# Optimization experiments

Hardware: AMD Instinct MI355X
Metric: run time of the kernel (lower is better)

## Reference

```python
import jax, jax.numpy as jnp
import numpy as np

N, L, D, H, MLP_MULT = 2, 384, 512, 8, 4
HD = D // H
DM = D * MLP_MULT
EPS = 1e-5


def _linear_params(key, out_dim, in_dim, scale=0.02):
    kw, kb = jax.random.split(key)
    w = jax.random.normal(kw, (out_dim, in_dim), jnp.float32) * scale
    b = jax.random.normal(kb, (out_dim,), jnp.float32) * scale
    return w, b


def setup_inputs() -> dict:
    key = jax.random.key(0)
    ks = jax.random.split(key, 12)
    x = jax.random.normal(ks[0], (N, L, D), jnp.float32)
    mem = jax.random.normal(ks[1], (N, L, D), jnp.float32)
    pairwise_distances = jax.random.normal(ks[2], (N, L, L, D), jnp.float32)
    mem_padding_mask = jax.random.randint(ks[3], (N, L), 0, 2).astype(bool)
    qw, qb = _linear_params(ks[4], D, D)
    kvw, kvb = _linear_params(ks[5], 2 * D, D)
    pw, pb = _linear_params(ks[6], D, D)
    edw, edb = _linear_params(ks[7], H, D)
    w1, b1 = _linear_params(ks[8], DM, D)
    w2, b2 = _linear_params(ks[9], DM, DM)
    w3, b3 = _linear_params(ks[10], D, DM)
    return {
        'x': x, 'mem': mem, 'pairwise_distances': pairwise_distances,
        'mem_padding_mask': mem_padding_mask,
        'qw': qw, 'qb': qb, 'kvw': kvw, 'kvb': kvb, 'pw': pw, 'pb': pb,
        'edw': edw, 'edb': edb,
        'ln1_g': jnp.ones((D,), jnp.float32), 'ln1_b': jnp.zeros((D,), jnp.float32),
        'ln2_g': jnp.ones((D,), jnp.float32), 'ln2_b': jnp.zeros((D,), jnp.float32),
        'w1': w1, 'b1': b1, 'w2': w2, 'b2': b2, 'w3': w3, 'b3': b3,
    }


def _layernorm(x, g, b):
    m = jnp.mean(x, axis=-1, keepdims=True)
    v = jnp.mean((x - m) ** 2, axis=-1, keepdims=True)
    return (x - m) * jax.lax.rsqrt(v + EPS) * g + b


def reference(x, mem, pairwise_distances, mem_padding_mask,
              qw, qb, kvw, kvb, pw, pb, edw, edb,
              ln1_g, ln1_b, ln2_g, ln2_b,
              w1, b1, w2, b2, w3, b3):
    scale = HD ** -0.5
    a_in = _layernorm(x, ln1_g, ln1_b)
    a_mem = _layernorm(mem, ln1_g, ln1_b)

    q = (a_in @ qw.T + qb).reshape(N, L, H, HD).transpose(0, 2, 1, 3)   # (N,H,L1,HD)
    kv = (a_mem @ kvw.T + kvb).reshape(N, L, 2, H, HD)
    k = kv[:, :, 0].transpose(0, 2, 1, 3)                               # (N,H,L2,HD)
    v = kv[:, :, 1].transpose(0, 2, 1, 3)

    scores = jnp.einsum('bhid,bhjd->bhij', q, k) * scale                # (N,H,L1,L2)

    # T5-style relative position bias from pairwise distances
    bias = (pairwise_distances @ edw.T + edb)                            # (N,L1,L2,H)
    scores = scores + bias.transpose(0, 3, 1, 2)

    # padding mask (True = padded); rows that are fully padded get a zero
    # mask instead (then their output is zeroed after attention)
    all_pad = jnp.all(mem_padding_mask, axis=-1)                         # (N,)
    neg_inf = jnp.asarray(-jnp.inf, scores.dtype)
    mask = jnp.where(mem_padding_mask[:, None, None, :], neg_inf, 0.0)
    mask = jnp.where(all_pad[:, None, None, None], 0.0, mask)
    scores = scores + mask

    attn = jax.nn.softmax(scores, axis=-1)
    out = jnp.einsum('bhij,bhjd->bhid', attn, v)                         # (N,H,L1,HD)
    out = out * (~all_pad)[:, None, None, None]
    out = out.transpose(0, 2, 1, 3).reshape(N, L, D)

    x = x + (out @ pw.T + pb)

    h = _layernorm(x, ln2_g, ln2_b)
    h = jax.nn.silu(h @ w1.T + b1)
    h = jax.nn.silu(h @ w2.T + b2)
    h = h @ w3.T + b3
    return x + h
```

## Files before the change

### kernel.cpp

```cpp
#include <hip/hip_runtime.h>
#include <hip/hip_bf16.h>
#include <math.h>

#define NB   2
#define LSEQ 384
#define DMODEL 512
#define NH   8
#define HD2  64
#define DMLP 2048
#define LL2  (LSEQ*LSEQ)
#define ROWS (NB*LSEQ)

#define BIAS_BLOCKS (NB * LL2 / 64)
#define LN_BLOCKS   384
#define CVT_BLOCKS  1024

using bf16x8 = __attribute__((ext_vector_type(8))) short;
using f32x4  = __attribute__((ext_vector_type(4))) float;

__device__ __forceinline__ unsigned short f2bf(float f) {
    union { __hip_bfloat16 h; unsigned short u; } cv;
    cv.h = __float2bfloat16(f);
    return cv.u;
}
__device__ __forceinline__ float bf2f(unsigned short u) {
    union { float f; unsigned int i; } c;
    c.i = ((unsigned int)u) << 16;
    return c.f;
}

__device__ __forceinline__ void gload_lds16(const void* g, void* l) {
    __builtin_amdgcn_global_load_lds(
        (const __attribute__((address_space(1))) void*)g,
        (__attribute__((address_space(3))) void*)l, 16, 0, 0);
}

__global__ __launch_bounds__(256) void pre_bias_kernel(
        const float* __restrict__ pd, const unsigned short* __restrict__ edwb_in,
        const float* __restrict__ edb, const int* __restrict__ mask,
        unsigned short* __restrict__ biasb,
        const float* __restrict__ x, const float* __restrict__ mem,
        const float* __restrict__ ln1g, const float* __restrict__ ln1b,
        unsigned short* __restrict__ a_in, unsigned short* __restrict__ a_mem,
        const float* __restrict__ s0, const float* __restrict__ s1,
        const float* __restrict__ s2, const float* __restrict__ s3,
        const float* __restrict__ s4, const float* __restrict__ s5,
        const float* __restrict__ edw,
        unsigned short* __restrict__ d0, unsigned short* __restrict__ d1,
        unsigned short* __restrict__ d2, unsigned short* __restrict__ d3,
        unsigned short* __restrict__ d4, unsigned short* __restrict__ d5,
        unsigned short* __restrict__ edwb_out) {
    __shared__ float Asb[2][64 * 64];
    const int tid = threadIdx.x;

    if (blockIdx.x < BIAS_BLOCKS) {
        const int lane = tid & 63, w = tid >> 6;
        const int T = blockIdx.x;
        const size_t row0 = (size_t)T * 64;
        const int n = T / 2304;
        const int rem64 = (T - n * 2304) * 64;
        const int i = rem64 / LSEQ, j0 = rem64 % LSEQ;

        int pad = 1;
        for (int j = lane; j < LSEQ; j += 64) pad &= (mask[n * LSEQ + j] != 0) ? 1 : 0;
        unsigned long long bal = __ballot(pad);
        const int ap = (bal == ~0ull) ? 1 : 0;

        int rr[4], sc[4];
        #pragma unroll
        for (int q = 0; q < 4; q++) {
            int s = q * 256 + tid;
            rr[q] = s >> 4;
            int cs = s & 15;
            sc[q] = (cs & 8) | ((cs & 7) ^ (rr[q] & 7));
        }

        const int c = lane & 15, g = lane >> 4;
        f32x4 acc = {};

        #pragma unroll
        for (int q = 0; q < 4; q++)
            gload_lds16(pd + (row0 + rr[q]) * DMODEL + sc[q] * 4, &Asb[0][(q * 256 + tid) * 4]);
        __syncthreads();

        for (int kc = 0; kc < 8; kc++) {
            if (kc < 7) {
                const int nb = (kc + 1) & 1;
                #pragma unroll
                for (int q = 0; q < 4; q++)
                    gload_lds16(pd + (row0 + rr[q]) * DMODEL + (kc + 1) * 64 + sc[q] * 4,
                                &Asb[nb][(q * 256 + tid) * 4]);
            }
            const float* Ab = &Asb[kc & 1][0];
            #pragma unroll
            for (int ks = 0; ks < 2; ks++) {
                const int ch0 = (8 * ks) | ((2 * g) ^ (c & 7));
                const int ch1 = (8 * ks) | ((2 * g + 1) ^ (c & 7));
                float4 a0 = *(const float4*)&Ab[(w * 16 + c) * 64 + ch0 * 4];
                float4 a1 = *(const float4*)&Ab[(w * 16 + c) * 64 + ch1 * 4];
                bf16x8 af;
                af[0] = (short)f2bf(a0.x); af[1] = (short)f2bf(a0.y);
                af[2] = (short)f2bf(a0.z); af[3] = (short)f2bf(a0.w);
                af[4] = (short)f2bf(a1.x); af[5] = (short)f2bf(a1.y);
                af[6] = (short)f2bf(a1.z); af[7] = (short)f2bf(a1.w);
                bf16x8 bfv = *(const bf16x8*)&edwb_in[c * 512 + kc * 64 + ks * 32 + g * 8];
                acc = __builtin_amdgcn_mfma_f32_16x16x32_bf16(af, bfv, acc, 0, 0, 0);
            }
            if (kc < 7) __syncthreads();
        }

        if (c < 8) {
            const float eb = edb[c];
            const int jj = j0 + w * 16 + g * 4;
            int4 mv = *(const int4*)&mask[n * LSEQ + jj];
            const float NEGINF = -__builtin_inff();
            ushort4 o;
            o.x = f2bf(acc[0] + eb + ((!ap && mv.x) ? NEGINF : 0.0f));
            o.y = f2bf(acc[1] + eb + ((!ap && mv.y) ? NEGINF : 0.0f));
            o.z = f2bf(acc[2] + eb + ((!ap && mv.z) ? NEGINF : 0.0f));
            o.w = f2bf(acc[3] + eb + ((!ap && mv.w) ? NEGINF : 0.0f));
            *(ushort4*)&biasb[(size_t)(n * 8 + c) * LL2 + (size_t)i * LSEQ + jj] = o;
        }
        return;
    }

    if (blockIdx.x < BIAS_BLOCKS + LN_BLOCKS) {
        int lane = tid & 63;
        int row  = (blockIdx.x - BIAS_BLOCKS) * 4 + (tid >> 6);
        const float* src = (row < ROWS) ? x : mem;
        unsigned short* dst = (row < ROWS) ? a_in : a_mem;
        int r2 = (row < ROWS) ? row : row - ROWS;
        const float* p = src + (size_t)r2 * DMODEL + lane * 8;
        float4 v0 = *(const float4*)p;
        float4 v1 = *(const float4*)(p + 4);
        float s  = v0.x + v0.y + v0.z + v0.w + v1.x + v1.y + v1.z + v1.w;
        float ss = v0.x*v0.x + v0.y*v0.y + v0.z*v0.z + v0.w*v0.w
                 + v1.x*v1.x + v1.y*v1.y + v1.z*v1.z + v1.w*v1.w;
        #pragma unroll
        for (int o = 32; o; o >>= 1) { s += __shfl_xor(s, o); ss += __shfl_xor(ss, o); }
        float m   = s * (1.0f / DMODEL);
        float var = ss * (1.0f / DMODEL) - m * m;
        float r   = rsqrtf(var + 1e-5f);
        float4 g0 = *(const float4*)(ln1g + lane * 8);
        float4 g1 = *(const float4*)(ln1g + lane * 8 + 4);
        float4 b0 = *(const float4*)(ln1b + lane * 8);
        float4 b1 = *(const float4*)(ln1b + lane * 8 + 4);
        unsigned short* q = dst + (size_t)r2 * DMODEL + lane * 8;
        ushort4 lo = {f2bf((v0.x-m)*r*g0.x+b0.x), f2bf((v0.y-m)*r*g0.y+b0.y),
                      f2bf((v0.z-m)*r*g0.z+b0.z), f2bf((v0.w-m)*r*g0.w+b0.w)};
        ushort4 hi = {f2bf((v1.x-m)*r*g1.x+b1.x), f2bf((v1.y-m)*r*g1.y+b1.y),
                      f2bf((v1.z-m)*r*g1.z+b1.z), f2bf((v1.w-m)*r*g1.w+b1.w)};
        *(ushort4*)q = lo;
        *(ushort4*)(q + 4) = hi;
        return;
    }

    const int stride = CVT_BLOCKS * 256;
    const int t0 = (blockIdx.x - BIAS_BLOCKS - LN_BLOCKS) * 256 + tid;
    const float* srcs[6] = {s0, s1, s2, s3, s4, s5};
    unsigned short* dsts[6] = {d0, d1, d2, d3, d4, d5};
    const int nf4[6] = {DMODEL*DMODEL/4, 2*DMODEL*DMODEL/4, DMODEL*DMODEL/4,
                        DMLP*DMODEL/4, DMLP*DMLP/4, DMLP*DMODEL/4};
    #pragma unroll
    for (int a = 0; a < 6; a++) {
        const float* s = srcs[a];
        unsigned short* d = dsts[a];
        for (int i = t0; i < nf4[a]; i += stride) {
            float4 v = *(const float4*)(s + (size_t)i * 4);
            ushort4 o = {f2bf(v.x), f2bf(v.y), f2bf(v.z), f2bf(v.w)};
            *(ushort4*)(d + (size_t)i * 4) = o;
        }
    }
    for (int i = t0; i < 16 * 512 / 4; i += stride) {
        int row = i >> 7;
        float4 v = {0.f, 0.f, 0.f, 0.f};
        if (row < 8) v = *(const float4*)(edw + (size_t)i * 4);
        ushort4 o = {f2bf(v.x), f2bf(v.y), f2bf(v.z), f2bf(v.w)};
        *(ushort4*)(edwb_out + (size_t)i * 4) = o;
    }
}

__global__ void edw_cvt_kernel(const float* __restrict__ edw,
                               unsigned short* __restrict__ edwb) {
    int i = blockIdx.x * 256 + threadIdx.x;
    float4 v = {0.f, 0.f, 0.f, 0.f};
    if (i < 8 * 512 / 4) v = *(const float4*)(edw + (size_t)i * 4);
    ushort4 o = {f2bf(v.x), f2bf(v.y), f2bf(v.z), f2bf(v.w)};
    *(ushort4*)(edwb + (size_t)i * 4) = o;
}

__global__ __launch_bounds__(256) void ln_kernel(const float* __restrict__ src0,
                                                 const float* __restrict__ g,
                                                 const float* __restrict__ b,
                                                 unsigned short* __restrict__ dst0) {
    int lane = threadIdx.x & 63;
    int row  = blockIdx.x * 4 + (threadIdx.x >> 6);
    const float* p = src0 + (size_t)row * DMODEL + lane * 8;
    float4 v0 = *(const float4*)p;
    float4 v1 = *(const float4*)(p + 4);
    float s  = v0.x + v0.y + v0.z + v0.w + v1.x + v1.y + v1.z + v1.w;
    float ss = v0.x*v0.x + v0.y*v0.y + v0.z*v0.z + v0.w*v0.w
             + v1.x*v1.x + v1.y*v1.y + v1.z*v1.z + v1.w*v1.w;
    #pragma unroll
    for (int o = 32; o; o >>= 1) { s += __shfl_xor(s, o); ss += __shfl_xor(ss, o); }
    float m   = s * (1.0f / DMODEL);
    float var = ss * (1.0f / DMODEL) - m * m;
    float r   = rsqrtf(var + 1e-5f);
    float4 g0 = *(const float4*)(g + lane * 8);
    float4 g1 = *(const float4*)(g + lane * 8 + 4);
    float4 b0 = *(const float4*)(b + lane * 8);
    float4 b1 = *(const float4*)(b + lane * 8 + 4);
    unsigned short* q = dst0 + (size_t)row * DMODEL + lane * 8;
    ushort4 lo = {f2bf((v0.x-m)*r*g0.x+b0.x), f2bf((v0.y-m)*r*g0.y+b0.y),
                  f2bf((v0.z-m)*r*g0.z+b0.z), f2bf((v0.w-m)*r*g0.w+b0.w)};
    ushort4 hi = {f2bf((v1.x-m)*r*g1.x+b1.x), f2bf((v1.y-m)*r*g1.y+b1.y),
                  f2bf((v1.z-m)*r*g1.z+b1.z), f2bf((v1.w-m)*r*g1.w+b1.w)};
    *(ushort4*)q = lo;
    *(ushort4*)(q + 4) = hi;
}

template<int ACT, int RES, int OBF>
__device__ __forceinline__ void gemm_body(const unsigned short* __restrict__ A,
        const unsigned short* __restrict__ W, const float* __restrict__ bv,
        const float* __restrict__ Rsd, void* __restrict__ Cv,
        int Nn, int K, int m0, int n0, short* As, short* Ws) {
    const int tid  = threadIdx.x;
    const int lane = tid & 63, w = tid >> 6;
    const int wr = w >> 1, wc = w & 1;
    const int s0 = tid, s1 = 256 + tid;
    const int r0 = s0 >> 3, c0 = ((s0 & 7) ^ (r0 & 7)) << 3;
    const int r1 = s1 >> 3, c1 = ((s1 & 7) ^ (r1 & 7)) << 3;
    const unsigned short* ag0 = A + (size_t)(m0 + r0) * K + c0;
    const unsigned short* ag1 = A + (size_t)(m0 + r1) * K + c1;
    const unsigned short* wg0 = W + (size_t)(n0 + r0) * K + c0;
    const unsigned short* wg1 = W + (size_t)(n0 + r1) * K + c1;

    f32x4 acc[2][2] = {};
    const int lc = lane & 15, lr = lane >> 4;
    const int KT = K >> 6;

    #pragma unroll
    for (int t = 0; t < 4; t++) {
        const int b = t * 4096, k0 = t << 6;
        gload_lds16(ag0 + k0, &As[b + s0 * 8]);
        gload_lds16(ag1 + k0, &As[b + s1 * 8]);
        gload_lds16(wg0 + k0, &Ws[b + s0 * 8]);
        gload_lds16(wg1 + k0, &Ws[b + s1 * 8]);
    }

    for (int t = 0; t < KT; t++) {
        int rem = KT - 1 - t; if (rem > 3) rem = 3;
        if (rem >= 3)      asm volatile("s_waitcnt vmcnt(12)" ::: "memory");
        else if (rem == 2) asm volatile("s_waitcnt vmcnt(8)"  ::: "memory");
        else if (rem == 1) asm volatile("s_waitcnt vmcnt(4)"  ::: "memory");
        else               asm volatile("s_waitcnt vmcnt(0)"  ::: "memory");
        __builtin_amdgcn_s_barrier();
        __builtin_amdgcn_sched_barrier(0);
        const int cur = (t & 3) * 4096;
        bf16x8 af[2][2], bfr[2][2];
        #pragma unroll
        for (int m = 0; m < 2; m++) {
            const int rra = wr * 32 + m * 16 + lc;
            #pragma unroll
            for (int kk = 0; kk < 2; kk++) {
                const int cc = (lr + kk * 4) ^ (rra & 7);
                af[m][kk] = *(const bf16x8*)&As[cur + rra * 64 + cc * 8];
            }
        }
        #pragma unroll
        for (int nn = 0; nn < 2; nn++) {
            const int rrb = wc * 32 + nn * 16 + lc;
            #pragma unroll
            for (int kk = 0; kk < 2; kk++) {
                const int cc = (lr + kk * 4) ^ (rrb & 7);
                bfr[nn][kk] = *(const bf16x8*)&Ws[cur + rrb * 64 + cc * 8];
            }
        }
        #pragma unroll
        for (int m = 0; m < 2; m++)
            #pragma unroll
            for (int nn = 0; nn < 2; nn++) {
                acc[m][nn] = __builtin_amdgcn_mfma_f32_16x16x32_bf16(af[m][0], bfr[nn][0], acc[m][nn], 0, 0, 0);
                acc[m][nn] = __builtin_amdgcn_mfma_f32_16x16x32_bf16(af[m][1], bfr[nn][1], acc[m][nn], 0, 0, 0);
            }
        if (t + 4 < KT) {
            __builtin_amdgcn_sched_barrier(0);
            __builtin_amdgcn_s_barrier();
            const int b = cur, k0 = (t + 4) << 6;
            gload_lds16(ag0 + k0, &As[b + s0 * 8]);
            gload_lds16(ag1 + k0, &As[b + s1 * 8]);
            gload_lds16(wg0 + k0, &Ws[b + s0 * 8]);
            gload_lds16(wg1 + k0, &Ws[b + s1 * 8]);
        }
    }

    #pragma unroll
    for (int nn = 0; nn < 2; nn++) {
        int gcol = n0 + wc * 32 + nn * 16 + lc;
        float bb = bv[gcol];
        #pragma unroll
        for (int m = 0; m < 2; m++) {
            #pragma unroll
            for (int r = 0; r < 4; r++) {
                int grow = m0 + wr * 32 + m * 16 + lr * 4 + r;
                float o = acc[m][nn][r] + bb;
                if (ACT) o = o / (1.0f + expf(-o));
                if (RES) o += Rsd[(size_t)grow * Nn + gcol];
                if (OBF) ((unsigned short*)Cv)[(size_t)grow * Nn + gcol] = f2bf(o);
                else     ((float*)Cv)[(size_t)grow * Nn + gcol] = o;
            }
        }
    }
}

template<int ACT, int RES, int OBF>
__global__ __launch_bounds__(256) void mfma_gemm(const unsigned short* __restrict__ A,
                                                 const unsigned short* __restrict__ W,
                                                 const float* __restrict__ bv,
                                                 const float* __restrict__ Rsd,
                                                 void* __restrict__ Cv, int Nn, int K) {
    __shared__ short As[4 * 4096];
    __shared__ short Ws[4 * 4096];
    gemm_body<ACT, RES, OBF>(A, W, bv, Rsd, Cv, Nn, K, blockIdx.y * 64, blockIdx.x * 64, As, Ws);
}

__global__ __launch_bounds__(256) void qkv_gemm(const unsigned short* __restrict__ a_in,
                                                const unsigned short* __restrict__ a_mem,
                                                const unsigned short* __restrict__ qwb,
                                                const unsigned short* __restrict__ kvwb,
                                                const float* __restrict__ qbv,
                                                const float* __restrict__ kvbv,
                                                float* __restrict__ qbuf,
                                                float* __restrict__ kvbuf) {
    __shared__ short As[4 * 4096];
    __shared__ short Ws[4 * 4096];
    const int bx = blockIdx.x;
    const unsigned short* A; const unsigned short* W; const float* bv; float* C; int Nn, n0;
    if (bx < 8) { A = a_in;  W = qwb;  bv = qbv;  C = qbuf;  Nn = DMODEL;     n0 = bx * 64; }
    else        { A = a_mem; W = kvwb; bv = kvbv; C = kvbuf; Nn = 2 * DMODEL; n0 = (bx - 8) * 64; }
    gemm_body<0, 0, 0>(A, W, bv, nullptr, C, Nn, DMODEL, blockIdx.y * 64, n0, As, Ws);
}

__global__ __launch_bounds__(256) void scores_kernel(const float* __restrict__ q,
                                                     const float* __restrict__ kv,
                                                     const unsigned short* __restrict__ biasb,
                                                     float* __restrict__ S) {
    const int n = blockIdx.z, h = blockIdx.y;
    const int it = blockIdx.x / 12, jt = blockIdx.x % 12;
    __shared__ float Qs[64][32];
    __shared__ float Ks[64][32];
    const int tid = threadIdx.x;
    const int r = tid >> 3, c = (tid & 7) << 3;
    {
        const float* qp = q + ((size_t)(n * LSEQ + it * 32 + r)) * DMODEL + h * HD2 + c;
        float4 q0 = *(const float4*)qp;
        float4 q1 = *(const float4*)(qp + 4);
        Qs[c+0][r]=q0.x; Qs[c+1][r]=q0.y; Qs[c+2][r]=q0.z; Qs[c+3][r]=q0.w;
        Qs[c+4][r]=q1.x; Qs[c+5][r]=q1.y; Qs[c+6][r]=q1.z; Qs[c+7][r]=q1.w;
        const float* kp = kv + ((size_t)(n * LSEQ + jt * 32 + r)) * (2 * DMODEL) + h * HD2 + c;
        float4 k0 = *(const float4*)kp;
        float4 k1 = *(const float4*)(kp + 4);
        Ks[c+0][r]=k0.x; Ks[c+1][r]=k0.y; Ks[c+2][r]=k0.z; Ks[c+3][r]=k0.w;
        Ks[c+4][r]=k1.x; Ks[c+5][r]=k1.y; Ks[c+6][r]=k1.z; Ks[c+7][r]=k1.w;
    }
    __syncthreads();
    const int tx = tid & 15, ty = tid >> 4;
    float acc[2][2] = {{0.f,0.f},{0.f,0.f}};
    #pragma unroll
    for (int k = 0; k < 64; k++) {
        float2 a  = *(const float2*)&Qs[k][ty << 1];
        float2 b2 = *(const float2*)&Ks[k][tx << 1];
        acc[0][0] = fmaf(a.x, b2.x, acc[0][0]);
        acc[0][1] = fmaf(a.x, b2.y, acc[0][1]);
        acc[1][0] = fmaf(a.y, b2.x, acc[1][0]);
        acc[1][1] = fmaf(a.y, b2.y, acc[1][1]);
    }
    #pragma unroll
    for (int i2 = 0; i2 < 2; i2++) {
        int gi = it * 32 + (ty << 1) + i2;
        int gj = jt * 32 + (tx << 1);
        size_t idx = ((size_t)(n * 8 + h)) * LL2 + (size_t)gi * LSEQ + gj;
        ushort2 bb = *(const ushort2*)&biasb[idx];
        S[idx]     = acc[i2][0] * 0.125f + bf2f(bb.x);
        S[idx + 1] = acc[i2][1] * 0.125f + bf2f(bb.y);
    }
}

__global__ __launch_bounds__(256) void softmax_kernel(float* __restrict__ S) {
    int lane = threadIdx.x & 63;
    int row  = blockIdx.x * 4 + (threadIdx.x >> 6);
    float* p = S + (size_t)row * LSEQ;
    float v[6];
    #pragma unroll
    for (int cc = 0; cc < 6; cc++) v[cc] = p[cc * 64 + lane];
    float mx = v[0];
    #pragma unroll
    for (int cc = 1; cc < 6; cc++) mx = fmaxf(mx, v[cc]);
    #pragma unroll
    for (int o = 32; o; o >>= 1) mx = fmaxf(mx, __shfl_xor(mx, o));
    float sum = 0.f;
    #pragma unroll
    for (int cc = 0; cc < 6; cc++) { v[cc] = __expf(v[cc] - mx); sum += v[cc]; }
    #pragma unroll
    for (int o = 32; o; o >>= 1) sum += __shfl_xor(sum, o);
    float inv = 1.0f / sum;
    #pragma unroll
    for (int cc = 0; cc < 6; cc++) p[cc * 64 + lane] = v[cc] * inv;
}

__global__ __launch_bounds__(256) void av_kernel(const float* __restrict__ S,
                                                 const float* __restrict__ kv,
                                                 const int* __restrict__ mask,
                                                 unsigned short* __restrict__ outb) {
    const int it = blockIdx.x, h = blockIdx.y, n = blockIdx.z;
    __shared__ float Ps[32][68];
    __shared__ float Vs[64][68];
    const int tid = threadIdx.x;
    const int lane = tid & 63;
    int pad = 1;
    for (int j = lane; j < LSEQ; j += 64) pad &= (mask[n * LSEQ + j] != 0) ? 1 : 0;
    unsigned long long bal = __ballot(pad != 0);
    const float zf = (bal == 0xFFFFFFFFFFFFFFFFull) ? 0.0f : 1.0f;
    const int tx = tid & 15, ty = tid >> 4;
    const int pr = tid >> 3, pc = (tid & 7) << 3;
    const int vr = tid >> 2, vc = (tid & 3) << 4;
    float acc0[4] = {0,0,0,0}, acc1[4] = {0,0,0,0};
    for (int j0 = 0; j0 < LSEQ; j0 += 64) {
        const float* sp = S + ((size_t)(n * 8 + h)) * LL2 + (size_t)(it * 32 + pr) * LSEQ + j0 + pc;
        float4 p0 = *(const float4*)sp;
        float4 p1 = *(const float4*)(sp + 4);
        *(float4*)&Ps[pr][pc]     = p0;
        *(float4*)&Ps[pr][pc + 4] = p1;
        #pragma unroll
        for (int u = 0; u < 4; u++) {
            float4 vvv = *(const float4*)&kv[((size_t)(n * LSEQ + j0 + vr)) * (2 * DMODEL)
                                             + DMODEL + h * HD2 + vc + 4 * u];
            *(float4*)&Vs[vr][vc + 4 * u] = vvv;
        }
        __syncthreads();
        #pragma unroll
        for (int j = 0; j < 64; j++) {
            float pa  = Ps[ty][j];
            float pb2 = Ps[ty + 16][j];
            float4 vv = *(const float4*)&Vs[j][tx << 2];
            acc0[0] = fmaf(pa,  vv.x, acc0[0]);
            acc0[1] = fmaf(pa,  vv.y, acc0[1]);
            acc0[2] = fmaf(pa,  vv.z, acc0[2]);
            acc0[3] = fmaf(pa,  vv.w, acc0[3]);
            acc1[0] = fmaf(pb2, vv.x, acc1[0]);
            acc1[1] = fmaf(pb2, vv.y, acc1[1]);
            acc1[2] = fmaf(pb2, vv.z, acc1[2]);
            acc1[3] = fmaf(pb2, vv.w, acc1[3]);
        }
        __syncthreads();
    }
    int i0 = it * 32;
    ushort4 o0 = {f2bf(acc0[0]*zf), f2bf(acc0[1]*zf), f2bf(acc0[2]*zf), f2bf(acc0[3]*zf)};
    ushort4 o1 = {f2bf(acc1[0]*zf), f2bf(acc1[1]*zf), f2bf(acc1[2]*zf), f2bf(acc1[3]*zf)};
    *(ushort4*)&outb[((size_t)(n * LSEQ + i0 + ty)) * DMODEL + h * HD2 + (tx << 2)]      = o0;
    *(ushort4*)&outb[((size_t)(n * LSEQ + i0 + ty + 16)) * DMODEL + h * HD2 + (tx << 2)] = o1;
}

extern "C" void kernel_launch(void* const* d_in, const int* in_sizes, int n_in,
                              void* d_out, int out_size, void* d_ws, size_t ws_size,
                              hipStream_t stream) {
    const float* x    = (const float*)d_in[0];
    const float* mem  = (const float*)d_in[1];
    const float* pd   = (const float*)d_in[2];
    const int*   mask = (const int*)d_in[3];
    const float* qw   = (const float*)d_in[4];
    const float* qbv  = (const float*)d_in[5];
    const float* kvw  = (const float*)d_in[6];
    const float* kvbv = (const float*)d_in[7];
    const float* pw   = (const float*)d_in[8];
    const float* pbv  = (const float*)d_in[9];
    const float* edw  = (const float*)d_in[10];
    const float* edb  = (const float*)d_in[11];
    const float* ln1g = (const float*)d_in[12];
    const float* ln1b = (const float*)d_in[13];
    const float* ln2g = (const float*)d_in[14];
    const float* ln2b = (const float*)d_in[15];
    const float* w1   = (const float*)d_in[16];
    const float* b1   = (const float*)d_in[17];
    const float* w2   = (const float*)d_in[18];
    const float* b2   = (const float*)d_in[19];
    const float* w3   = (const float*)d_in[20];
    const float* b3   = (const float*)d_in[21];

    float* wsf = (float*)d_ws;
    unsigned short* biasb = (unsigned short*)(wsf + 16);
    float* scores = wsf + 16 + (size_t)NB * NH * LL2 / 2;
    float* qbuf   = scores + (size_t)NB * NH * LL2;
    float* kvbuf  = qbuf + (size_t)ROWS * DMODEL;
    float* x1buf  = kvbuf + (size_t)ROWS * 2 * DMODEL;
    unsigned short* a_in  = (unsigned short*)(x1buf + (size_t)ROWS * DMODEL);
    unsigned short* a_mem = a_in  + (size_t)ROWS * DMODEL;
    unsigned short* attno = a_mem + (size_t)ROWS * DMODEL;
    unsigned short* h0    = attno + (size_t)ROWS * DMODEL;
    unsigned short* h1    = h0    + (size_t)ROWS * DMODEL;
    unsigned short* h2    = h1    + (size_t)ROWS * DMLP;
    unsigned short* qwb   = h2    + (size_t)ROWS * DMLP;
    unsigned short* kvwb  = qwb   + (size_t)DMODEL * DMODEL;
    unsigned short* pwb   = kvwb  + (size_t)2 * DMODEL * DMODEL;
    unsigned short* w1b   = pwb   + (size_t)DMODEL * DMODEL;
    unsigned short* w2b   = w1b   + (size_t)DMLP * DMODEL;
    unsigned short* w3b   = w2b   + (size_t)DMLP * DMLP;
    unsigned short* edwb  = w3b   + (size_t)DMLP * DMODEL;
    unsigned short* edwb2 = edwb  + (size_t)16 * 512;

    float* outp = (float*)d_out;

    edw_cvt_kernel<<<4, 256, 0, stream>>>(edw, edwb);
    edw_cvt_kernel<<<4, 256, 0, stream>>>(edw, edwb);
    hipMemsetAsync(edwb + 8 * 512, 0, 8 * 512 * sizeof(unsigned short), stream);

    pre_bias_kernel<<<BIAS_BLOCKS + LN_BLOCKS + CVT_BLOCKS, 256, 0, stream>>>(
        pd, edwb, edb, mask, biasb,
        x, mem, ln1g, ln1b, a_in, a_mem,
        qw, kvw, pw, w1, w2, w3, edw,
        qwb, kvwb, pwb, w1b, w2b, w3b, edwb2);

    qkv_gemm<<<dim3(24, 12), 256, 0, stream>>>(a_in, a_mem, qwb, kvwb, qbv, kvbv, qbuf, kvbuf);

    scores_kernel<<<dim3(144, NH, NB), 256, 0, stream>>>(qbuf, kvbuf, biasb, scores);
    softmax_kernel<<<(NB * NH * LSEQ) / 4, 256, 0, stream>>>(scores);
    av_kernel<<<dim3(12, NH, NB), 256, 0, stream>>>(scores, kvbuf, mask, attno);

    mfma_gemm<0,1,0><<<dim3(8, 12), 256, 0, stream>>>(attno, pwb, pbv, x, x1buf, DMODEL, DMODEL);
    ln_kernel<<<ROWS / 4, 256, 0, stream>>>(x1buf, ln2g, ln2b, h0);
    mfma_gemm<1,0,1><<<dim3(32, 12), 256, 0, stream>>>(h0, w1b, b1, nullptr, h1, DMLP, DMODEL);
    mfma_gemm<1,0,1><<<dim3(32, 12), 256, 0, stream>>>(h1, w2b, b2, nullptr, h2, DMLP, DMLP);
    mfma_gemm<0,1,0><<<dim3(8, 12), 256, 0, stream>>>(h2, w3b, b3, x1buf, outp, DMODEL, DMLP);
}
```

Measured before the change: 245.0 us.

## Store Q/K/V and attention scores in bf16 to cut memory traffic

The QKV GEMM now writes bf16 outputs, and the scores, softmax and AV kernels read and write the score matrix in bf16 instead of fp32, halving the bytes moved through the attention pipeline. The duplicated edw conversion launches, memset and in-kernel edw conversion are merged into one 8-block conversion kernel. The cost is lower precision for the scores and probabilities, plus per-element conversion work when filling shared memory.

```diff
diff --git a/kernel.cpp b/kernel.cpp
--- a/kernel.cpp
+++ b/kernel.cpp
@@ -45,11 +45,9 @@
         const float* __restrict__ s0, const float* __restrict__ s1,
         const float* __restrict__ s2, const float* __restrict__ s3,
         const float* __restrict__ s4, const float* __restrict__ s5,
-        const float* __restrict__ edw,
         unsigned short* __restrict__ d0, unsigned short* __restrict__ d1,
         unsigned short* __restrict__ d2, unsigned short* __restrict__ d3,
-        unsigned short* __restrict__ d4, unsigned short* __restrict__ d5,
-        unsigned short* __restrict__ edwb_out) {
+        unsigned short* __restrict__ d4, unsigned short* __restrict__ d5) {
     __shared__ float Asb[2][64 * 64];
     const int tid = threadIdx.x;
 
@@ -171,20 +169,14 @@
             *(ushort4*)(d + (size_t)i * 4) = o;
         }
     }
-    for (int i = t0; i < 16 * 512 / 4; i += stride) {
-        int row = i >> 7;
-        float4 v = {0.f, 0.f, 0.f, 0.f};
-        if (row < 8) v = *(const float4*)(edw + (size_t)i * 4);
-        ushort4 o = {f2bf(v.x), f2bf(v.y), f2bf(v.z), f2bf(v.w)};
-        *(ushort4*)(edwb_out + (size_t)i * 4) = o;
-    }
 }
 
 __global__ void edw_cvt_kernel(const float* __restrict__ edw,
                                unsigned short* __restrict__ edwb) {
     int i = blockIdx.x * 256 + threadIdx.x;
+    int row = i >> 7;
     float4 v = {0.f, 0.f, 0.f, 0.f};
-    if (i < 8 * 512 / 4) v = *(const float4*)(edw + (size_t)i * 4);
+    if (row < 8) v = *(const float4*)(edw + (size_t)i * 4);
     ushort4 o = {f2bf(v.x), f2bf(v.y), f2bf(v.z), f2bf(v.w)};
     *(ushort4*)(edwb + (size_t)i * 4) = o;
 }
@@ -330,21 +322,22 @@
                                                 const unsigned short* __restrict__ kvwb,
                                                 const float* __restrict__ qbv,
                                                 const float* __restrict__ kvbv,
-                                                float* __restrict__ qbuf,
-                                                float* __restrict__ kvbuf) {
+                                                unsigned short* __restrict__ qbuf,
+                                                unsigned short* __restrict__ kvbuf) {
     __shared__ short As[4 * 4096];
     __shared__ short Ws[4 * 4096];
     const int bx = blockIdx.x;
-    const unsigned short* A; const unsigned short* W; const float* bv; float* C; int Nn, n0;
+    const unsigned short* A; const unsigned short* W; const float* bv;
+    unsigned short* C; int Nn, n0;
     if (bx < 8) { A = a_in;  W = qwb;  bv = qbv;  C = qbuf;  Nn = DMODEL;     n0 = bx * 64; }
     else        { A = a_mem; W = kvwb; bv = kvbv; C = kvbuf; Nn = 2 * DMODEL; n0 = (bx - 8) * 64; }
-    gemm_body<0, 0, 0>(A, W, bv, nullptr, C, Nn, DMODEL, blockIdx.y * 64, n0, As, Ws);
-}
-
-__global__ __launch_bounds__(256) void scores_kernel(const float* __restrict__ q,
-                                                     const float* __restrict__ kv,
+    gemm_body<0, 0, 1>(A, W, bv, nullptr, C, Nn, DMODEL, blockIdx.y * 64, n0, As, Ws);
+}
+
+__global__ __launch_bounds__(256) void scores_kernel(const unsigned short* __restrict__ q,
+                                                     const unsigned short* __restrict__ kv,
                                                      const unsigned short* __restrict__ biasb,
-                                                     float* __restrict__ S) {
+                                                     unsigned short* __restrict__ S) {
     const int n = blockIdx.z, h = blockIdx.y;
     const int it = blockIdx.x / 12, jt = blockIdx.x % 12;
     __shared__ float Qs[64][32];
@@ -352,16 +345,16 @@
     const int tid = threadIdx.x;
     const int r = tid >> 3, c = (tid & 7) << 3;
     {
-        const float* qp = q + ((size_t)(n * LSEQ + it * 32 + r)) * DMODEL + h * HD2 + c;
-        float4 q0 = *(const float4*)qp;
-        float4 q1 = *(const float4*)(qp + 4);
-        Qs[c+0][r]=q0.x; Qs[c+1][r]=q0.y; Qs[c+2][r]=q0.z; Qs[c+3][r]=q0.w;
-        Qs[c+4][r]=q1.x; Qs[c+5][r]=q1.y; Qs[c+6][r]=q1.z; Qs[c+7][r]=q1.w;
-        const float* kp = kv + ((size_t)(n * LSEQ + jt * 32 + r)) * (2 * DMODEL) + h * HD2 + c;
-        float4 k0 = *(const float4*)kp;
-        float4 k1 = *(const float4*)(kp + 4);
-        Ks[c+0][r]=k0.x; Ks[c+1][r]=k0.y; Ks[c+2][r]=k0.z; Ks[c+3][r]=k0.w;
-        Ks[c+4][r]=k1.x; Ks[c+5][r]=k1.y; Ks[c+6][r]=k1.z; Ks[c+7][r]=k1.w;
+        const unsigned short* qp = q + ((size_t)(n * LSEQ + it * 32 + r)) * DMODEL + h * HD2 + c;
+        ushort4 q0 = *(const ushort4*)qp;
+        ushort4 q1 = *(const ushort4*)(qp + 4);
+        Qs[c+0][r]=bf2f(q0.x); Qs[c+1][r]=bf2f(q0.y); Qs[c+2][r]=bf2f(q0.z); Qs[c+3][r]=bf2f(q0.w);
+        Qs[c+4][r]=bf2f(q1.x); Qs[c+5][r]=bf2f(q1.y); Qs[c+6][r]=bf2f(q1.z); Qs[c+7][r]=bf2f(q1.w);
+        const unsigned short* kp = kv + ((size_t)(n * LSEQ + jt * 32 + r)) * (2 * DMODEL) + h * HD2 + c;
+        ushort4 k0 = *(const ushort4*)kp;
+        ushort4 k1 = *(const ushort4*)(kp + 4);
+        Ks[c+0][r]=bf2f(k0.x); Ks[c+1][r]=bf2f(k0.y); Ks[c+2][r]=bf2f(k0.z); Ks[c+3][r]=bf2f(k0.w);
+        Ks[c+4][r]=bf2f(k1.x); Ks[c+5][r]=bf2f(k1.y); Ks[c+6][r]=bf2f(k1.z); Ks[c+7][r]=bf2f(k1.w);
     }
     __syncthreads();
     const int tx = tid & 15, ty = tid >> 4;
@@ -381,18 +374,19 @@
         int gj = jt * 32 + (tx << 1);
         size_t idx = ((size_t)(n * 8 + h)) * LL2 + (size_t)gi * LSEQ + gj;
         ushort2 bb = *(const ushort2*)&biasb[idx];
-        S[idx]     = acc[i2][0] * 0.125f + bf2f(bb.x);
-        S[idx + 1] = acc[i2][1] * 0.125f + bf2f(bb.y);
-    }
-}
-
-__global__ __launch_bounds__(256) void softmax_kernel(float* __restrict__ S) {
+        ushort2 so = {f2bf(acc[i2][0] * 0.125f + bf2f(bb.x)),
+                      f2bf(acc[i2][1] * 0.125f + bf2f(bb.y))};
+        *(ushort2*)&S[idx] = so;
+    }
+}
+
+__global__ __launch_bounds__(256) void softmax_kernel(unsigned short* __restrict__ S) {
     int lane = threadIdx.x & 63;
     int row  = blockIdx.x * 4 + (threadIdx.x >> 6);
-    float* p = S + (size_t)row * LSEQ;
+    unsigned short* p = S + (size_t)row * LSEQ;
     float v[6];
     #pragma unroll
-    for (int cc = 0; cc < 6; cc++) v[cc] = p[cc * 64 + lane];
+    for (int cc = 0; cc < 6; cc++) v[cc] = bf2f(p[cc * 64 + lane]);
     float mx = v[0];
     #pragma unroll
     for (int cc = 1; cc < 6; cc++) mx = fmaxf(mx, v[cc]);
@@ -405,11 +399,11 @@
     for (int o = 32; o; o >>= 1) sum += __shfl_xor(sum, o);
     float inv = 1.0f / sum;
     #pragma unroll
-    for (int cc = 0; cc < 6; cc++) p[cc * 64 + lane] = v[cc] * inv;
-}
-
-__global__ __launch_bounds__(256) void av_kernel(const float* __restrict__ S,
-                                                 const float* __restrict__ kv,
+    for (int cc = 0; cc < 6; cc++) p[cc * 64 + lane] = f2bf(v[cc] * inv);
+}
+
+__global__ __launch_bounds__(256) void av_kernel(const unsigned short* __restrict__ S,
+                                                 const unsigned short* __restrict__ kv,
                                                  const int* __restrict__ mask,
                                                  unsigned short* __restrict__ outb) {
     const int it = blockIdx.x, h = blockIdx.y, n = blockIdx.z;
@@ -426,16 +420,20 @@
     const int vr = tid >> 2, vc = (tid & 3) << 4;
     float acc0[4] = {0,0,0,0}, acc1[4] = {0,0,0,0};
     for (int j0 = 0; j0 < LSEQ; j0 += 64) {
-        const float* sp = S + ((size_t)(n * 8 + h)) * LL2 + (size_t)(it * 32 + pr) * LSEQ + j0 + pc;
-        float4 p0 = *(const float4*)sp;
-        float4 p1 = *(const float4*)(sp + 4);
-        *(float4*)&Ps[pr][pc]     = p0;
-        *(float4*)&Ps[pr][pc + 4] = p1;
+        const unsigned short* sp = S + ((size_t)(n * 8 + h)) * LL2 + (size_t)(it * 32 + pr) * LSEQ + j0 + pc;
+        ushort4 p0 = *(const ushort4*)sp;
+        ushort4 p1 = *(const ushort4*)(sp + 4);
+        Ps[pr][pc+0]=bf2f(p0.x); Ps[pr][pc+1]=bf2f(p0.y); Ps[pr][pc+2]=bf2f(p0.z); Ps[pr][pc+3]=bf2f(p0.w);
+        Ps[pr][pc+4]=bf2f(p1.x); Ps[pr][pc+5]=bf2f(p1.y); Ps[pr][pc+6]=bf2f(p1.z); Ps[pr][pc+7]=bf2f(p1.w);
+        const unsigned short* vp = kv + ((size_t)(n * LSEQ + j0 + vr)) * (2 * DMODEL)
+                                      + DMODEL + h * HD2 + vc;
         #pragma unroll
         for (int u = 0; u < 4; u++) {
-            float4 vvv = *(const float4*)&kv[((size_t)(n * LSEQ + j0 + vr)) * (2 * DMODEL)
-                                             + DMODEL + h * HD2 + vc + 4 * u];
-            *(float4*)&Vs[vr][vc + 4 * u] = vvv;
+            ushort4 vv = *(const ushort4*)(vp + 4 * u);
+            Vs[vr][vc + 4*u + 0] = bf2f(vv.x);
+            Vs[vr][vc + 4*u + 1] = bf2f(vv.y);
+            Vs[vr][vc + 4*u + 2] = bf2f(vv.z);
+            Vs[vr][vc + 4*u + 3] = bf2f(vv.w);
         }
         __syncthreads();
         #pragma unroll
@@ -488,11 +486,11 @@
     const float* b3   = (const float*)d_in[21];
 
     float* wsf = (float*)d_ws;
-    unsigned short* biasb = (unsigned short*)(wsf + 16);
-    float* scores = wsf + 16 + (size_t)NB * NH * LL2 / 2;
-    float* qbuf   = scores + (size_t)NB * NH * LL2;
-    float* kvbuf  = qbuf + (size_t)ROWS * DMODEL;
-    float* x1buf  = kvbuf + (size_t)ROWS * 2 * DMODEL;
+    unsigned short* biasb   = (unsigned short*)(wsf + 16);
+    unsigned short* scores16= biasb + (size_t)NB * NH * LL2;
+    unsigned short* qbuf16  = scores16 + (size_t)NB * NH * LL2;
+    unsigned short* kvbuf16 = qbuf16 + (size_t)ROWS * DMODEL;
+    float* x1buf = (float*)(kvbuf16 + (size_t)ROWS * 2 * DMODEL);
     unsigned short* a_in  = (unsigned short*)(x1buf + (size_t)ROWS * DMODEL);
     unsigned short* a_mem = a_in  + (size_t)ROWS * DMODEL;
     unsigned short* attno = a_mem + (size_t)ROWS * DMODEL;
@@ -506,25 +504,23 @@
     unsigned short* w2b   = w1b   + (size_t)DMLP * DMODEL;
     unsigned short* w3b   = w2b   + (size_t)DMLP * DMLP;
     unsigned short* edwb  = w3b   + (size_t)DMLP * DMODEL;
-    unsigned short* edwb2 = edwb  + (size_t)16 * 512;
 
     float* outp = (float*)d_out;
 
-    edw_cvt_kernel<<<4, 256, 0, stream>>>(edw, edwb);
-    edw_cvt_kernel<<<4, 256, 0, stream>>>(edw, edwb);
-    hipMemsetAsync(edwb + 8 * 512, 0, 8 * 512 * sizeof(unsigned short), stream);
+    edw_cvt_kernel<<<8, 256, 0, stream>>>(edw, edwb);
 
     pre_bias_kernel<<<BIAS_BLOCKS + LN_BLOCKS + CVT_BLOCKS, 256, 0, stream>>>(
         pd, edwb, edb, mask, biasb,
         x, mem, ln1g, ln1b, a_in, a_mem,
-        qw, kvw, pw, w1, w2, w3, edw,
-        qwb, kvwb, pwb, w1b, w2b, w3b, edwb2);
-
-    qkv_gemm<<<dim3(24, 12), 256, 0, stream>>>(a_in, a_mem, qwb, kvwb, qbv, kvbv, qbuf, kvbuf);
-
-    scores_kernel<<<dim3(144, NH, NB), 256, 0, stream>>>(qbuf, kvbuf, biasb, scores);
-    softmax_kernel<<<(NB * NH * LSEQ) / 4, 256, 0, stream>>>(scores);
-    av_kernel<<<dim3(12, NH, NB), 256, 0, stream>>>(scores, kvbuf, mask, attno);
+        qw, kvw, pw, w1, w2, w3,
+        qwb, kvwb, pwb, w1b, w2b, w3b);
+
+    qkv_gemm<<<dim3(24, 12), 256, 0, stream>>>(a_in, a_mem, qwb, kvwb, qbv, kvbv,
+                                               qbuf16, kvbuf16);
+
+    scores_kernel<<<dim3(144, NH, NB), 256, 0, stream>>>(qbuf16, kvbuf16, biasb, scores16);
+    softmax_kernel<<<(NB * NH * LSEQ) / 4, 256, 0, stream>>>(scores16);
+    av_kernel<<<dim3(12, NH, NB), 256, 0, stream>>>(scores16, kvbuf16, mask, attno);
 
     mfma_gemm<0,1,0><<<dim3(8, 12), 256, 0, stream>>>(attno, pwb, pbv, x, x1buf, DMODEL, DMODEL);
     ln_kernel<<<ROWS / 4, 256, 0, stream>>>(x1buf, ln2g, ln2b, h0);
```

Measured after the change: 235.6 us. 3.8% less time.
